# Optimization experiments

Hardware: AMD Instinct MI355X
Metric: run time of the kernel (lower is better)

The kernel has to match this reference:

```python
import jax, jax.numpy as jnp
import numpy as np

DIM = 1024
HEADS = 16
BS = 2
N = 2048

def setup_inputs() -> dict:
    key = jax.random.key(0)
    ks = jax.random.split(key, 7)
    s = 1.0 / np.sqrt(DIM)
    seq = jax.random.normal(ks[0], (BS, N, DIM), dtype=jnp.float32)
    attn_mask = jax.random.normal(ks[1], (N, N), dtype=jnp.float32)
    Wqkv = jax.random.normal(ks[2], (DIM, 3 * DIM), dtype=jnp.float32) * s
    W1 = jax.random.normal(ks[3], (DIM, 2 * DIM), dtype=jnp.float32) * s
    b1 = jnp.zeros((2 * DIM,), dtype=jnp.float32)
    W2 = jax.random.normal(ks[4], (2 * DIM, DIM), dtype=jnp.float32) * (1.0 / np.sqrt(2 * DIM))
    b2 = jnp.zeros((DIM,), dtype=jnp.float32)
    return {"seq": seq, "attn_mask": attn_mask, "Wqkv": Wqkv,
            "W1": W1, "b1": b1, "W2": W2, "b2": b2}

def reference(seq, attn_mask, Wqkv, W1, b1, W2, b2):
    bs, n, dim = seq.shape
    h = HEADS
    hd = dim // h
    x = seq @ Wqkv                                  # [bs, n, 3*dim]
    q, k, v = jnp.split(x, 3, axis=-1)
    q = q.reshape(bs, n, h, hd)
    k = k.reshape(bs, n, h, hd)
    v = v.reshape(bs, n, h, hd)
    scores = jnp.einsum('bnhd,bmhd->bhnm', q, k) / (hd ** 0.5)
    scores = scores + attn_mask[None, None, :, :]
    attn = jax.nn.softmax(scores, axis=-1)
    out = jnp.einsum('bhnm,bmhd->bnhd', attn, v).reshape(bs, n, dim)
    # SiLU FFN (dropout inactive at inference)
    hid = jax.nn.silu(out @ W1 + b1)
    return hid @ W2 + b2
```

## Files before the change

kernel.cpp:

```cpp
#include <hip/hip_runtime.h>
#include <math.h>

#define SEQ   2048
#define NHEAD 16
#define HD    64
#define BSZ   2
#define MTOT  (BSZ*SEQ)

#define LOG2E    1.4426950408889634f
#define C_SCALE  0.18033688011112043f
#define C_MOFF  -23.083120654223414f

typedef __bf16 bf16x8 __attribute__((ext_vector_type(8)));
typedef short  s16x8  __attribute__((ext_vector_type(8)));
typedef short  s16x4  __attribute__((ext_vector_type(4)));
typedef float  f32x4  __attribute__((ext_vector_type(4)));

__device__ __forceinline__ short f2bf(float x) {
    unsigned u = __builtin_bit_cast(unsigned, x);
    u = (u + 0x7fffu + ((u >> 16) & 1u)) >> 16;
    return (short)u;
}
__device__ __forceinline__ float bf2f(short h) {
    unsigned u = ((unsigned)(unsigned short)h) << 16;
    return __builtin_bit_cast(float, u);
}

__device__ __forceinline__ void gl_lds16(const short* g, short* l) {
    __builtin_amdgcn_global_load_lds(
        (const __attribute__((address_space(1))) unsigned int*)g,
        (__attribute__((address_space(3))) unsigned int*)l, 16, 0, 0);
}

__device__ __forceinline__ void tsplit_tile(const float* __restrict__ W,
    short* __restrict__ Th, short* __restrict__ Tl,
    int K, int N, int k0, int n0, float (*T)[33], int t)
{
    {
        const int kl = t >> 3;
        const int nl = (t & 7) * 4;
        const float4 v = *(const float4*)&W[(size_t)(k0 + kl) * N + n0 + nl];
        T[nl + 0][kl] = v.x; T[nl + 1][kl] = v.y;
        T[nl + 2][kl] = v.z; T[nl + 3][kl] = v.w;
    }
    __syncthreads();
    {
        const int nl = t >> 3;
        const int kl = (t & 7) * 4;
        s16x4 h, l;
        #pragma unroll
        for (int c = 0; c < 4; ++c) {
            const float x = T[nl][kl + c];
            const short hb = f2bf(x);
            h[c] = hb;
            l[c] = f2bf(x - bf2f(hb));
        }
        const size_t o = (size_t)(n0 + nl) * K + k0 + kl;
        *(s16x4*)&Th[o] = h;
        *(s16x4*)&Tl[o] = l;
    }
}

__global__ __launch_bounds__(256)
void prep_kernel(const float* __restrict__ seq, short* __restrict__ seqh,
                 const float* __restrict__ Wqkv, short* __restrict__ WtQh, short* __restrict__ WtQl,
                 const float* __restrict__ W1, short* __restrict__ Wt1h, short* __restrict__ Wt1l)
{
    __shared__ float T[32][33];
    const int t = threadIdx.x;
    const int bid = blockIdx.x;
    if (bid < 1024) {
        const size_t base = (size_t)bid * 4096 + (size_t)t * 16;
        #pragma unroll
        for (int c = 0; c < 4; ++c) {
            const float4 v = *(const float4*)&seq[base + c * 4];
            s16x4 h;
            h[0] = f2bf(v.x); h[1] = f2bf(v.y); h[2] = f2bf(v.z); h[3] = f2bf(v.w);
            *(s16x4*)&seqh[base + c * 4] = h;
        }
    } else if (bid < 4096) {
        const int idx = bid - 1024;
        tsplit_tile(Wqkv, WtQh, WtQl, 1024, 3072, (idx & 31) * 32, (idx >> 5) * 32, T, t);
    } else {
        const int idx = bid - 4096;
        tsplit_tile(W1, Wt1h, Wt1l, 1024, 2048, (idx & 31) * 32, (idx >> 5) * 32, T, t);
    }
}

__global__ __launch_bounds__(256)
void util_kernel(const short* __restrict__ Vnat, short* __restrict__ Vth,
                 const float* __restrict__ W2, short* __restrict__ Wt2h, short* __restrict__ Wt2l)
{
    __shared__ float T[32][33];
    const int t = threadIdx.x;
    const int bid = blockIdx.x;
    if (bid < 4096) {
        short (*TT)[36] = (short(*)[36])T;
        const int r0 = (bid & 127) * 32;
        const int f0 = (bid >> 7) * 32;
        {
            const int rl = t >> 3;
            const int fl = (t & 7) * 4;
            const s16x4 v = *(const s16x4*)&Vnat[(size_t)(r0 + rl) * 1024 + f0 + fl];
            TT[fl + 0][rl] = v[0]; TT[fl + 1][rl] = v[1];
            TT[fl + 2][rl] = v[2]; TT[fl + 3][rl] = v[3];
        }
        __syncthreads();
        {
            const int fl = t >> 3;
            const int rl = (t & 7) * 4;
            s16x4 o;
            o[0] = TT[fl][rl + 0]; o[1] = TT[fl][rl + 1];
            o[2] = TT[fl][rl + 2]; o[3] = TT[fl][rl + 3];
            *(s16x4*)&Vth[(size_t)(f0 + fl) * 4096 + r0 + rl] = o;
        }
    } else {
        const int idx = bid - 4096;
        tsplit_tile(W2, Wt2h, Wt2l, 2048, 1024, (idx & 63) * 32, (idx >> 6) * 32, T, t);
    }
}

template<int ACT, int OMODE, int VT, int NB>
__global__ __launch_bounds__(256, 2)
void gemm2(const short* __restrict__ Ahg,
           const short* __restrict__ Bhg, const short* __restrict__ Blg,
           const float* __restrict__ bias,
           float* __restrict__ Cf, short* __restrict__ Chg, short* __restrict__ Clg,
           short* __restrict__ Vng,
           int M, int N, int K, int NOUT)
{
    constexpr int NJ = NB / 32;
    __shared__ short AhL[128 * 32];
    __shared__ short BhL[NB * 32];
    __shared__ short BlL[NB * 32];

    const int t    = threadIdx.x;
    const int m0   = blockIdx.y * 128;
    const int n0   = blockIdx.x * NB;
    const int wave = t >> 6;
    const int lane = t & 63;
    const int r    = lane & 15;
    const int qd   = lane >> 4;
    const int wm   = (wave & 1) * 64;
    const int wn   = (wave >> 1) * (NB / 2);

    f32x4 acc[4][NJ];
    #pragma unroll
    for (int i = 0; i < 4; ++i)
        #pragma unroll
        for (int j = 0; j < NJ; ++j) acc[i][j] = (f32x4){0.f, 0.f, 0.f, 0.f};

    for (int k0 = 0; k0 < K; k0 += 32) {
        __syncthreads();
        #pragma unroll
        for (int s = 0; s < 2; ++s) {
            const int p    = wave * 2 + s;
            const int srow = p * 16 + (lane >> 2);
            const int sg   = (lane & 3) ^ ((srow >> 1) & 3);
            const size_t ga = (size_t)(m0 + srow) * K + k0 + sg * 8;
            gl_lds16(&Ahg[ga], &AhL[p * 512]);
        }
        #pragma unroll
        for (int s = 0; s < NB / 64; ++s) {
            const int p    = wave * (NB / 64) + s;
            const int srow = p * 16 + (lane >> 2);
            const int sg   = (lane & 3) ^ ((srow >> 1) & 3);
            const size_t gb = (size_t)(n0 + srow) * K + k0 + sg * 8;
            gl_lds16(&Bhg[gb], &BhL[p * 512]);
            gl_lds16(&Blg[gb], &BlL[p * 512]);
        }
        __syncthreads();

        bf16x8 afh[4], bfh[NJ], bfl[NJ];
        #pragma unroll
        for (int i = 0; i < 4; ++i) {
            const int row = wm + i * 16 + r;
            const int oa = row * 32 + ((qd ^ ((row >> 1) & 3)) * 8);
            afh[i] = __builtin_bit_cast(bf16x8, *(const s16x8*)&AhL[oa]);
        }
        #pragma unroll
        for (int j = 0; j < NJ; ++j) {
            const int row = wn + j * 16 + r;
            const int ob = row * 32 + ((qd ^ ((row >> 1) & 3)) * 8);
            bfh[j] = __builtin_bit_cast(bf16x8, *(const s16x8*)&BhL[ob]);
            bfl[j] = __builtin_bit_cast(bf16x8, *(const s16x8*)&BlL[ob]);
        }

        #pragma unroll
        for (int i = 0; i < 4; ++i)
            #pragma unroll
            for (int j = 0; j < NJ; ++j) {
                acc[i][j] = __builtin_amdgcn_mfma_f32_16x16x32_bf16(afh[i], bfh[j], acc[i][j], 0, 0, 0);
                acc[i][j] = __builtin_amdgcn_mfma_f32_16x16x32_bf16(afh[i], bfl[j], acc[i][j], 0, 0, 0);
            }
    }

    #pragma unroll
    for (int i = 0; i < 4; ++i)
        #pragma unroll
        for (int j = 0; j < NJ; ++j) {
            const int col = n0 + wn + j * 16 + r;
            if (VT && col >= 2048) {
                #pragma unroll
                for (int g = 0; g < 4; ++g) {
                    const int row = m0 + wm + i * 16 + qd * 4 + g;
                    Vng[(size_t)row * 1024 + (col - 2048)] = f2bf(acc[i][j][g]);
                }
            } else {
                const float bv = bias ? bias[col] : 0.f;
                #pragma unroll
                for (int g = 0; g < 4; ++g) {
                    const int row = m0 + wm + i * 16 + qd * 4 + g;
                    float x = acc[i][j][g] + bv;
                    if (ACT == 1) x = x / (1.0f + __expf(-x));
                    if (OMODE == 0) {
                        Cf[(size_t)row * NOUT + col] = x;
                    } else if (OMODE == 1) {
                        const short hb = f2bf(x);
                        Chg[(size_t)row * NOUT + col] = hb;
                        Clg[(size_t)row * NOUT + col] = f2bf(x - bf2f(hb));
                    } else {
                        Chg[(size_t)row * NOUT + col] = f2bf(x);
                    }
                }
            }
        }
}

__global__ __launch_bounds__(256, 2)
void attn_mfma3(const short* __restrict__ Xh, const short* __restrict__ Xl,
                const short* __restrict__ Vth, const float* __restrict__ mask,
                short* __restrict__ atth)
{
    __shared__ short KhL[2 * 64 * 64];
    __shared__ short KlL[2 * 64 * 64];
    __shared__ short VhL[2 * 64 * 64];
    __shared__ short PhL[128 * 64];

    const int t    = threadIdx.x;
    const int lane = t & 63;
    const int w    = t >> 6;
    const int r    = lane & 15;
    const int qd   = lane >> 4;
    const int b    = blockIdx.x >> 4;
    const int h    = blockIdx.x & 15;
    const int q0   = blockIdx.y * 128;

    const int srow0 = (lane >> 3);
    const int sgx   = lane & 7;

    bf16x8 qh[2][2], ql[2][2];
    #pragma unroll
    for (int i = 0; i < 2; ++i) {
        const size_t qoff = (size_t)(b * SEQ + q0 + w * 32 + i * 16 + r) * 2048 + h * 64;
        #pragma unroll
        for (int ks = 0; ks < 2; ++ks) {
            qh[i][ks] = __builtin_bit_cast(bf16x8, *(const s16x8*)&Xh[qoff + ks * 32 + qd * 8]);
            ql[i][ks] = __builtin_bit_cast(bf16x8, *(const s16x8*)&Xl[qoff + ks * 32 + qd * 8]);
        }
    }

    s16x8 ones_s;
    #pragma unroll
    for (int c = 0; c < 8; ++c) ones_s[c] = (short)0x3F80;
    const bf16x8 ones = __builtin_bit_cast(bf16x8, ones_s);

    f32x4 O[2][4], Lac[2];
    #pragma unroll
    for (int i = 0; i < 2; ++i) {
        Lac[i] = (f32x4){0.f, 0.f, 0.f, 0.f};
        #pragma unroll
        for (int j = 0; j < 4; ++j) O[i][j] = (f32x4){0.f, 0.f, 0.f, 0.f};
    }

    auto stage = [&](int kt, int buf) {
        const int k0   = kt * 64;
        const int tok0 = b * SEQ + k0;
        const int bo   = buf * 4096;
        #pragma unroll
        for (int s = 0; s < 2; ++s) {
            const int p    = w * 2 + s;
            const int srow = p * 8 + srow0;
            const int sg   = sgx ^ (srow & 7);
            const size_t gk = (size_t)(tok0 + srow) * 2048 + 1024 + h * 64 + sg * 8;
            gl_lds16(&Xh[gk], &KhL[bo + p * 512]);
            gl_lds16(&Xl[gk], &KlL[bo + p * 512]);
            const size_t gv = (size_t)(h * 64 + srow) * 4096 + (size_t)b * SEQ + k0 + sg * 8;
            gl_lds16(&Vth[gv], &VhL[bo + p * 512]);
        }
    };

    stage(0, 0);

    for (int kt = 0; kt < SEQ / 64; ++kt) {
        const int cur = kt & 1;
        const int k0  = kt * 64;

        __syncthreads();
        if (kt + 1 < SEQ / 64) stage(kt + 1, 1 - cur);

        float mreg[2][4][4];
        #pragma unroll
        for (int i = 0; i < 2; ++i)
            #pragma unroll
            for (int g = 0; g < 4; ++g) {
                const size_t mrow = (size_t)(q0 + w * 32 + i * 16 + qd * 4 + g) * SEQ + k0;
                #pragma unroll
                for (int j = 0; j < 4; ++j)
                    mreg[i][g][j] = fmaf(mask[mrow + j * 16 + r], LOG2E, C_MOFF);
            }

        const int co = cur * 4096;
        f32x4 S[2][4];
        #pragma unroll
        for (int i = 0; i < 2; ++i)
            #pragma unroll
            for (int j = 0; j < 4; ++j) S[i][j] = (f32x4){0.f, 0.f, 0.f, 0.f};
        #pragma unroll
        for (int ks = 0; ks < 2; ++ks) {
            bf16x8 kfh[4], kfl[4];
            #pragma unroll
            for (int j = 0; j < 4; ++j) {
                const int row = j * 16 + r;
                const int off = co + row * 64 + (((ks * 4 + qd) ^ (row & 7)) * 8);
                kfh[j] = __builtin_bit_cast(bf16x8, *(const s16x8*)&KhL[off]);
                kfl[j] = __builtin_bit_cast(bf16x8, *(const s16x8*)&KlL[off]);
            }
            #pragma unroll
            for (int i = 0; i < 2; ++i)
                #pragma unroll
                for (int j = 0; j < 4; ++j) {
                    S[i][j] = __builtin_amdgcn_mfma_f32_16x16x32_bf16(qh[i][ks], kfh[j], S[i][j], 0, 0, 0);
                    S[i][j] = __builtin_amdgcn_mfma_f32_16x16x32_bf16(qh[i][ks], kfl[j], S[i][j], 0, 0, 0);
                    S[i][j] = __builtin_amdgcn_mfma_f32_16x16x32_bf16(ql[i][ks], kfh[j], S[i][j], 0, 0, 0);
                }
        }

        #pragma unroll
        for (int i = 0; i < 2; ++i)
            #pragma unroll
            for (int j = 0; j < 4; ++j)
                #pragma unroll
                for (int g = 0; g < 4; ++g)
                    S[i][j][g] = exp2f(fmaf(S[i][j][g], C_SCALE, mreg[i][g][j]));

        #pragma unroll
        for (int i = 0; i < 2; ++i)
            #pragma unroll
            for (int j = 0; j < 4; ++j)
                #pragma unroll
                for (int g = 0; g < 4; ++g) {
                    const int prow = w * 32 + i * 16 + qd * 4 + g;
                    const int gr   = (j * 2 + (r >> 3)) ^ ((prow >> 1) & 7);
                    PhL[prow * 64 + gr * 8 + (r & 7)] = f2bf(S[i][j][g]);
                }

        #pragma unroll
        for (int ks = 0; ks < 2; ++ks) {
            bf16x8 pfh[2], vfh[4];
            #pragma unroll
            for (int i = 0; i < 2; ++i) {
                const int row = w * 32 + i * 16 + r;
                pfh[i] = __builtin_bit_cast(bf16x8,
                    *(const s16x8*)&PhL[row * 64 + (((ks * 4 + qd) ^ ((row >> 1) & 7)) * 8)]);
            }
            #pragma unroll
            for (int j = 0; j < 4; ++j) {
                const int row = j * 16 + r;
                vfh[j] = __builtin_bit_cast(bf16x8,
                    *(const s16x8*)&VhL[co + row * 64 + (((ks * 4 + qd) ^ (row & 7)) * 8)]);
            }
            #pragma unroll
            for (int i = 0; i < 2; ++i) {
                Lac[i] = __builtin_amdgcn_mfma_f32_16x16x32_bf16(pfh[i], ones, Lac[i], 0, 0, 0);
                #pragma unroll
                for (int j = 0; j < 4; ++j)
                    O[i][j] = __builtin_amdgcn_mfma_f32_16x16x32_bf16(pfh[i], vfh[j], O[i][j], 0, 0, 0);
            }
        }
    }

    #pragma unroll
    for (int i = 0; i < 2; ++i)
        #pragma unroll
        for (int g = 0; g < 4; ++g) {
            const float inv = 1.0f / Lac[i][g];
            const size_t row = (size_t)(b * SEQ + q0 + w * 32 + i * 16 + qd * 4 + g);
            #pragma unroll
            for (int j = 0; j < 4; ++j)
                atth[row * 1024 + h * 64 + j * 16 + r] = f2bf(O[i][j][g] * inv);
        }
}

extern "C" void kernel_launch(void* const* d_in, const int* in_sizes, int n_in,
                              void* d_out, int out_size, void* d_ws, size_t ws_size,
                              hipStream_t stream)
{
    const float* seq  = (const float*)d_in[0];
    const float* mask = (const float*)d_in[1];
    const float* Wqkv = (const float*)d_in[2];
    const float* W1   = (const float*)d_in[3];
    const float* b1   = (const float*)d_in[4];
    const float* W2   = (const float*)d_in[5];
    const float* b2   = (const float*)d_in[6];
    float* out = (float*)d_out;

    const size_t MiB = 1048576;
    char* B = (char*)d_ws;
    short* Xh   = (short*)(B + 0);
    short* Xl   = (short*)(B + 16 * MiB);
    short* Vnat = (short*)(B + 32 * MiB);
    short* Wt1h = (short*)(B + 40 * MiB);
    short* Wt1l = (short*)(B + 44 * MiB);
    short* WtQh = (short*)(B + 48 * MiB);
    short* WtQl = (short*)(B + 54 * MiB);
    short* Vth  = (short*)(B + 48 * MiB);
    short* Wt2h = (short*)(B + 56 * MiB);
    short* Wt2l = (short*)(B + 60 * MiB);
    short* hidh = (short*)(B + 0);

    short* seqh = (short*)d_out;
    short* atth = (short*)d_out;

    prep_kernel<<<6144, 256, 0, stream>>>(seq, seqh, Wqkv, WtQh, WtQl, W1, Wt1h, Wt1l);

    gemm2<0, 1, 1, 128><<<dim3(3072 / 128, MTOT / 128), 256, 0, stream>>>(
        seqh, WtQh, WtQl, nullptr,
        nullptr, Xh, Xl, Vnat, MTOT, 3072, 1024, 2048);

    util_kernel<<<6144, 256, 0, stream>>>(Vnat, Vth, W2, Wt2h, Wt2l);

    attn_mfma3<<<dim3(BSZ * NHEAD, SEQ / 128), 256, 0, stream>>>(Xh, Xl, Vth, mask, atth);

    gemm2<1, 2, 0, 128><<<dim3(2048 / 128, MTOT / 128), 256, 0, stream>>>(
        atth, Wt1h, Wt1l, b1,
        nullptr, hidh, nullptr, nullptr, MTOT, 2048, 1024, 2048);

    gemm2<0, 0, 0, 64><<<dim3(1024 / 64, MTOT / 128), 256, 0, stream>>>(
        hidh, Wt2h, Wt2l, b2,
        out, nullptr, nullptr, nullptr, MTOT, 1024, 2048, 1024);
}
```

Baseline: 352.9 us.

## Load V fragments directly from global into registers, drop V LDS staging

V tiles are no longer staged through shared memory with async global-to-LDS copies. Each lane instead loads its V fragments straight from global memory into registers after the exp step. This frees 16 KB of LDS and allows launch bounds of 3 blocks per SM. The change also packs the P conversion with v_cvt_pk_bf16_f32 and raises wave priority around the MFMA blocks. The cost is that the V global loads are now exposed inside the loop instead of being double-buffered, and register pressure rises under the tighter occupancy bound.

```diff
diff --git a/kernel.cpp b/kernel.cpp
--- a/kernel.cpp
+++ b/kernel.cpp
@@ -24,6 +24,12 @@
 __device__ __forceinline__ float bf2f(short h) {
     unsigned u = ((unsigned)(unsigned short)h) << 16;
     return __builtin_bit_cast(float, u);
+}
+
+__device__ __forceinline__ unsigned cvt_pk_bf16(float a, float b) {
+    unsigned r;
+    asm("v_cvt_pk_bf16_f32 %0, %1, %2" : "=v"(r) : "v"(a), "v"(b));
+    return r;
 }
 
 __device__ __forceinline__ void gl_lds16(const short* g, short* l) {
@@ -227,14 +233,13 @@
         }
 }
 
-__global__ __launch_bounds__(256, 2)
+__global__ __launch_bounds__(256, 3)
 void attn_mfma3(const short* __restrict__ Xh, const short* __restrict__ Xl,
                 const short* __restrict__ Vth, const float* __restrict__ mask,
                 short* __restrict__ atth)
 {
     __shared__ short KhL[2 * 64 * 64];
     __shared__ short KlL[2 * 64 * 64];
-    __shared__ short VhL[2 * 64 * 64];
     __shared__ short PhL[128 * 64];
 
     const int t    = threadIdx.x;
@@ -285,12 +290,12 @@
             const size_t gk = (size_t)(tok0 + srow) * 2048 + 1024 + h * 64 + sg * 8;
             gl_lds16(&Xh[gk], &KhL[bo + p * 512]);
             gl_lds16(&Xl[gk], &KlL[bo + p * 512]);
-            const size_t gv = (size_t)(h * 64 + srow) * 4096 + (size_t)b * SEQ + k0 + sg * 8;
-            gl_lds16(&Vth[gv], &VhL[bo + p * 512]);
         }
     };
 
     stage(0, 0);
+
+    const size_t vbase = (size_t)(h * 64 + r) * 4096 + (size_t)b * SEQ;
 
     for (int kt = 0; kt < SEQ / 64; ++kt) {
         const int cur = kt & 1;
@@ -326,6 +331,7 @@
                 kfh[j] = __builtin_bit_cast(bf16x8, *(const s16x8*)&KhL[off]);
                 kfl[j] = __builtin_bit_cast(bf16x8, *(const s16x8*)&KlL[off]);
             }
+            __builtin_amdgcn_s_setprio(1);
             #pragma unroll
             for (int i = 0; i < 2; ++i)
                 #pragma unroll
@@ -334,6 +340,7 @@
                     S[i][j] = __builtin_amdgcn_mfma_f32_16x16x32_bf16(qh[i][ks], kfl[j], S[i][j], 0, 0, 0);
                     S[i][j] = __builtin_amdgcn_mfma_f32_16x16x32_bf16(ql[i][ks], kfh[j], S[i][j], 0, 0, 0);
                 }
+            __builtin_amdgcn_s_setprio(0);
         }
 
         #pragma unroll
@@ -344,16 +351,29 @@
                 for (int g = 0; g < 4; ++g)
                     S[i][j][g] = exp2f(fmaf(S[i][j][g], C_SCALE, mreg[i][g][j]));
 
+        s16x8 vreg[2][4];
+        #pragma unroll
+        for (int ks = 0; ks < 2; ++ks)
+            #pragma unroll
+            for (int j = 0; j < 4; ++j)
+                vreg[ks][j] = *(const s16x8*)&Vth[vbase + (size_t)(j * 16) * 4096
+                                                 + k0 + (ks * 4 + qd) * 8];
+
         #pragma unroll
         for (int i = 0; i < 2; ++i)
             #pragma unroll
-            for (int j = 0; j < 4; ++j)
+            for (int j = 0; j < 4; ++j) {
+                const unsigned pk01 = cvt_pk_bf16(S[i][j][0], S[i][j][1]);
+                const unsigned pk23 = cvt_pk_bf16(S[i][j][2], S[i][j][3]);
+                const short ph[4] = {(short)pk01, (short)(pk01 >> 16),
+                                     (short)pk23, (short)(pk23 >> 16)};
                 #pragma unroll
                 for (int g = 0; g < 4; ++g) {
                     const int prow = w * 32 + i * 16 + qd * 4 + g;
                     const int gr   = (j * 2 + (r >> 3)) ^ ((prow >> 1) & 7);
-                    PhL[prow * 64 + gr * 8 + (r & 7)] = f2bf(S[i][j][g]);
+                    PhL[prow * 64 + gr * 8 + (r & 7)] = ph[g];
                 }
+            }
 
         #pragma unroll
         for (int ks = 0; ks < 2; ++ks) {
@@ -365,11 +385,9 @@
                     *(const s16x8*)&PhL[row * 64 + (((ks * 4 + qd) ^ ((row >> 1) & 7)) * 8)]);
             }
             #pragma unroll
-            for (int j = 0; j < 4; ++j) {
-                const int row = j * 16 + r;
-                vfh[j] = __builtin_bit_cast(bf16x8,
-                    *(const s16x8*)&VhL[co + row * 64 + (((ks * 4 + qd) ^ (row & 7)) * 8)]);
-            }
+            for (int j = 0; j < 4; ++j)
+                vfh[j] = __builtin_bit_cast(bf16x8, vreg[ks][j]);
+            __builtin_amdgcn_s_setprio(1);
             #pragma unroll
             for (int i = 0; i < 2; ++i) {
                 Lac[i] = __builtin_amdgcn_mfma_f32_16x16x32_bf16(pfh[i], ones, Lac[i], 0, 0, 0);
@@ -377,6 +395,7 @@
                 for (int j = 0; j < 4; ++j)
                     O[i][j] = __builtin_amdgcn_mfma_f32_16x16x32_bf16(pfh[i], vfh[j], O[i][j], 0, 0, 0);
             }
+            __builtin_amdgcn_s_setprio(0);
         }
     }
 
```

After: 773.8 us. +119.3%, slower.

## Alias P tile onto current K buffers and raise MFMA priority in attention

Applied to the files above, without the earlier changes.

Merges the separate K-high, K-low, V and P shared arrays into one LDS block. The per-wave P tile now reuses the current stage's K buffers after a new barrier, which cuts LDS per block from 64 KB to 48 KB so more blocks can fit on a CU. Wraps the MFMA loops in s_setprio so waves issuing matrix ops get scheduling priority. The cost is an extra __syncthreads per key tile, and launch_bounds(256,2) may still cap how much occupancy the LDS saving can bring.

```diff
diff --git a/kernel.cpp b/kernel.cpp
--- a/kernel.cpp
+++ b/kernel.cpp
@@ -232,10 +232,7 @@
                 const short* __restrict__ Vth, const float* __restrict__ mask,
                 short* __restrict__ atth)
 {
-    __shared__ short KhL[2 * 64 * 64];
-    __shared__ short KlL[2 * 64 * 64];
-    __shared__ short VhL[2 * 64 * 64];
-    __shared__ short PhL[128 * 64];
+    __shared__ short SM[6 * 4096];
 
     const int t    = threadIdx.x;
     const int lane = t & 63;
@@ -283,14 +280,16 @@
             const int srow = p * 8 + srow0;
             const int sg   = sgx ^ (srow & 7);
             const size_t gk = (size_t)(tok0 + srow) * 2048 + 1024 + h * 64 + sg * 8;
-            gl_lds16(&Xh[gk], &KhL[bo + p * 512]);
-            gl_lds16(&Xl[gk], &KlL[bo + p * 512]);
+            gl_lds16(&Xh[gk], &SM[bo + p * 512]);
+            gl_lds16(&Xl[gk], &SM[8192 + bo + p * 512]);
             const size_t gv = (size_t)(h * 64 + srow) * 4096 + (size_t)b * SEQ + k0 + sg * 8;
-            gl_lds16(&Vth[gv], &VhL[bo + p * 512]);
+            gl_lds16(&Vth[gv], &SM[16384 + bo + p * 512]);
         }
     };
 
     stage(0, 0);
+
+    const int pbase_w = (w >> 1) * 8192 + (w & 1) * 2048;
 
     for (int kt = 0; kt < SEQ / 64; ++kt) {
         const int cur = kt & 1;
@@ -323,9 +322,10 @@
             for (int j = 0; j < 4; ++j) {
                 const int row = j * 16 + r;
                 const int off = co + row * 64 + (((ks * 4 + qd) ^ (row & 7)) * 8);
-                kfh[j] = __builtin_bit_cast(bf16x8, *(const s16x8*)&KhL[off]);
-                kfl[j] = __builtin_bit_cast(bf16x8, *(const s16x8*)&KlL[off]);
-            }
+                kfh[j] = __builtin_bit_cast(bf16x8, *(const s16x8*)&SM[off]);
+                kfl[j] = __builtin_bit_cast(bf16x8, *(const s16x8*)&SM[8192 + off]);
+            }
+            __builtin_amdgcn_s_setprio(1);
             #pragma unroll
             for (int i = 0; i < 2; ++i)
                 #pragma unroll
@@ -334,6 +334,7 @@
                     S[i][j] = __builtin_amdgcn_mfma_f32_16x16x32_bf16(qh[i][ks], kfl[j], S[i][j], 0, 0, 0);
                     S[i][j] = __builtin_amdgcn_mfma_f32_16x16x32_bf16(ql[i][ks], kfh[j], S[i][j], 0, 0, 0);
                 }
+            __builtin_amdgcn_s_setprio(0);
         }
 
         #pragma unroll
@@ -344,15 +345,18 @@
                 for (int g = 0; g < 4; ++g)
                     S[i][j][g] = exp2f(fmaf(S[i][j][g], C_SCALE, mreg[i][g][j]));
 
+        __syncthreads();
+
+        const int pb = co + pbase_w;
         #pragma unroll
         for (int i = 0; i < 2; ++i)
             #pragma unroll
             for (int j = 0; j < 4; ++j)
                 #pragma unroll
                 for (int g = 0; g < 4; ++g) {
-                    const int prow = w * 32 + i * 16 + qd * 4 + g;
-                    const int gr   = (j * 2 + (r >> 3)) ^ ((prow >> 1) & 7);
-                    PhL[prow * 64 + gr * 8 + (r & 7)] = f2bf(S[i][j][g]);
+                    const int lrow = i * 16 + qd * 4 + g;
+                    const int gr   = (j * 2 + (r >> 3)) ^ ((lrow >> 1) & 7);
+                    SM[pb + lrow * 64 + gr * 8 + (r & 7)] = f2bf(S[i][j][g]);
                 }
 
         #pragma unroll
@@ -360,16 +364,17 @@
             bf16x8 pfh[2], vfh[4];
             #pragma unroll
             for (int i = 0; i < 2; ++i) {
-                const int row = w * 32 + i * 16 + r;
+                const int lrow = i * 16 + r;
                 pfh[i] = __builtin_bit_cast(bf16x8,
-                    *(const s16x8*)&PhL[row * 64 + (((ks * 4 + qd) ^ ((row >> 1) & 7)) * 8)]);
+                    *(const s16x8*)&SM[pb + lrow * 64 + (((ks * 4 + qd) ^ ((lrow >> 1) & 7)) * 8)]);
             }
             #pragma unroll
             for (int j = 0; j < 4; ++j) {
                 const int row = j * 16 + r;
                 vfh[j] = __builtin_bit_cast(bf16x8,
-                    *(const s16x8*)&VhL[co + row * 64 + (((ks * 4 + qd) ^ (row & 7)) * 8)]);
-            }
+                    *(const s16x8*)&SM[16384 + co + row * 64 + (((ks * 4 + qd) ^ (row & 7)) * 8)]);
+            }
+            __builtin_amdgcn_s_setprio(1);
             #pragma unroll
             for (int i = 0; i < 2; ++i) {
                 Lac[i] = __builtin_amdgcn_mfma_f32_16x16x32_bf16(pfh[i], ones, Lac[i], 0, 0, 0);
@@ -377,6 +382,7 @@
                 for (int j = 0; j < 4; ++j)
                     O[i][j] = __builtin_amdgcn_mfma_f32_16x16x32_bf16(pfh[i], vfh[j], O[i][j], 0, 0, 0);
             }
+            __builtin_amdgcn_s_setprio(0);
         }
     }
 
```

After: 362.1 us. 2.6% more time.
